# Kernel optimization log

Hardware: AMD Instinct MI355X
Metric: run time of the kernel (lower is better)

Reference implementation:

```python
import jax, jax.numpy as jnp
import numpy as np


def lut_quantize(v, lut):
    """Nearest-neighbor LUT quantization with straight-through estimator.
    lut is sorted ascending; uses searchsorted (no [N, L] blowup)."""
    L = lut.shape[0]
    idx = jnp.clip(jnp.searchsorted(lut, v), 1, L - 1)
    left = jnp.take(lut, idx - 1)
    right = jnp.take(lut, idx)
    q = jnp.where(v - left <= right - v, left, right)
    return v + jax.lax.stop_gradient(q - v)


def mem_conv(x, w, b, lut):
    # memConv2d: weights/bias snapped to LUT levels, then standard 3x3 SAME conv (NCHW/OIHW)
    wq = lut_quantize(w, lut)
    bq = lut_quantize(b, lut)
    y = jax.lax.conv_general_dilated(x, wq, window_strides=(1, 1),
                                     padding=((1, 1), (1, 1)),
                                     dimension_numbers=('NCHW', 'OIHW', 'NCHW'))
    return y + bq[None, :, None, None]


def mem_linear(x, w, b, lut):
    # memLinear: torch-style weight (out, in)
    return x @ lut_quantize(w, lut).T + lut_quantize(b, lut)


def mem_relu(x, lut):
    # memReLu: ReLU followed by LUT quantization of the activation
    return lut_quantize(jnp.maximum(x, 0.0), lut)


def max_pool_2x2(x):
    return jax.lax.reduce_window(x, -jnp.inf, jax.lax.max,
                                 (1, 1, 2, 2), (1, 1, 2, 2), 'VALID')


def _forward(x, lut, w1, b1, w2, b2, w3, b3, w4, b4, w5, b5, w6, b6,
             fw1, fb1, fw2, fb2, fw3, fb3):
    x = mem_relu(mem_conv(x, w1, b1, lut), lut)
    x = mem_relu(mem_conv(x, w2, b2, lut), lut)
    x = max_pool_2x2(x)                      # [B,32,16,16]
    x = mem_relu(mem_conv(x, w3, b3, lut), lut)
    x = mem_relu(mem_conv(x, w4, b4, lut), lut)
    x = max_pool_2x2(x)                      # [B,64,8,8]
    x = mem_relu(mem_conv(x, w5, b5, lut), lut)
    x = mem_relu(mem_conv(x, w6, b6, lut), lut)
    x = max_pool_2x2(x)                      # [B,128,4,4]
    x = x.reshape(-1, 128 * 4 * 4)
    x = mem_relu(mem_linear(x, fw1, fb1, lut), lut)
    x = mem_relu(mem_linear(x, fw2, fb2, lut), lut)
    x = mem_linear(x, fw3, fb3, lut)
    return jax.nn.softmax(x, axis=1)


def setup_inputs() -> dict:
    key = jax.random.key(0)
    ks = jax.random.split(key, 20)
    B = 512
    lut = jnp.linspace(-4.0, 4.0, 129).astype(jnp.float32)

    def conv_w(k, co, ci):
        scale = np.sqrt(2.0 / (ci * 9)).astype(np.float32)
        return jax.random.normal(k, (co, ci, 3, 3), jnp.float32) * scale

    def lin_w(k, co, ci):
        scale = np.sqrt(2.0 / ci).astype(np.float32)
        return jax.random.normal(k, (co, ci), jnp.float32) * scale

    return {
        'x': jax.random.normal(ks[0], (B, 3, 32, 32), jnp.float32),
        'lut': lut,
        'w1': conv_w(ks[1], 32, 3),   'b1': jnp.zeros((32,), jnp.float32),
        'w2': conv_w(ks[2], 32, 32),  'b2': jnp.zeros((32,), jnp.float32),
        'w3': conv_w(ks[3], 64, 32),  'b3': jnp.zeros((64,), jnp.float32),
        'w4': conv_w(ks[4], 64, 64),  'b4': jnp.zeros((64,), jnp.float32),
        'w5': conv_w(ks[5], 128, 64), 'b5': jnp.zeros((128,), jnp.float32),
        'w6': conv_w(ks[6], 128, 128),'b6': jnp.zeros((128,), jnp.float32),
        'fw1': lin_w(ks[7], 512, 2048), 'fb1': jnp.zeros((512,), jnp.float32),
        'fw2': lin_w(ks[8], 128, 512),  'fb2': jnp.zeros((128,), jnp.float32),
        'fw3': lin_w(ks[9], 10, 128),   'fb3': jnp.zeros((10,), jnp.float32),
    }


def reference(x, lut, w1, b1, w2, b2, w3, b3, w4, b4, w5, b5, w6, b6,
              fw1, fb1, fw2, fb2, fw3, fb3):
    return _forward(x, lut, w1, b1, w2, b2, w3, b3, w4, b4, w5, b5, w6, b6,
                    fw1, fb1, fw2, fb2, fw3, fb3)
```

## Files before the change

kernel.cpp:

```cpp
#include <hip/hip_runtime.h>
#include <cstddef>


#define B_SZ 512
typedef unsigned int u32;
typedef __attribute__((ext_vector_type(4))) int i32x4;

__device__ __forceinline__ float lutq(float v) {
    float k = ceilf(v * 16.0f - 0.5f);
    k = fminf(64.0f, fmaxf(-64.0f, k));
    return k * 0.0625f;
}
__device__ __forceinline__ int kq(float x) {
    float kf = ceilf(x * 16.0f - 0.5f);
    kf = fminf(64.0f, fmaxf(-64.0f, kf));
    return (int)kf;
}
__device__ __forceinline__ u32 bmax4u(u32 a, u32 b) {
    u32 r = 0;
    #pragma unroll
    for (int j = 0; j < 4; ++j) {
        u32 x = (a >> (8 * j)) & 255u, y = (b >> (8 * j)) & 255u;
        r |= (x > y ? x : y) << (8 * j);
    }
    return r;
}

__device__ __forceinline__ void prep_conv_frag(const float* __restrict__ w, char* __restrict__ q,
                                               int i, int CI) {
    int NSTEP = (9 * CI + 63) / 64;
    int e = i & 15, t = i >> 4;
    int ln = t & 63, t2 = t >> 6;
    int s = t2 % NSTEP, co_tile = t2 / NSTEP;
    int k = s * 64 + ((ln >> 4) << 4) + e;
    int tap = k / CI, ci = k % CI;
    int co = co_tile * 16 + (ln & 15);
    int val = 0;
    if (tap < 9) val = kq(w[(co * CI + ci) * 9 + tap]);
    q[i] = (char)val;
}
__device__ __forceinline__ void prep_fc_frag(const float* __restrict__ w, char* __restrict__ q,
                                             int i, int K) {
    int S = K >> 6;
    int e = i & 15, t = i >> 4;
    int ln = t & 63, t2 = t >> 6;
    int s = t2 % S, n_tile = t2 / S;
    int n = n_tile * 16 + (ln & 15);
    int k = s * 64 + ((ln >> 4) << 4) + e;
    q[i] = (char)kq(w[(size_t)n * K + k]);
}

__global__ __launch_bounds__(256) void prep_weights(
    const float* __restrict__ w2, const float* __restrict__ w3, const float* __restrict__ w4,
    const float* __restrict__ w5, const float* __restrict__ w6,
    const float* __restrict__ fw1, const float* __restrict__ fw2,
    char* q2, char* q3, char* q4, char* q5, char* q6, char* qf1, char* qf2)
{
    int i = blockIdx.x * 256 + threadIdx.x;
    if (i < 10240)                  { prep_conv_frag(w2, q2, i, 32);  }
    else if ((i -= 10240) < 20480)  { prep_conv_frag(w3, q3, i, 32);  }
    else if ((i -= 20480) < 36864)  { prep_conv_frag(w4, q4, i, 64);  }
    else if ((i -= 36864) < 73728)  { prep_conv_frag(w5, q5, i, 64);  }
    else if ((i -= 73728) < 147456) { prep_conv_frag(w6, q6, i, 128); }
    else if ((i -= 147456) < 1048576){ prep_fc_frag(fw1, qf1, i, 2048); }
    else if ((i -= 1048576) < 65536) { prep_fc_frag(fw2, qf2, i, 512);  }
}

__global__ __launch_bounds__(256) void conv1_mem(
    const float* __restrict__ x, const float* __restrict__ w,
    const float* __restrict__ bias, char* __restrict__ out)
{
    __shared__ float s_w[3][9][16];
    __shared__ float s_b[16];
    __shared__ float s_in[3][10][34];
    const int tid = threadIdx.x;
    const int co0 = blockIdx.y * 16;
    const int b   = blockIdx.x >> 2;
    const int r0  = (blockIdx.x & 3) * 8;
    for (int i = tid; i < 432; i += 256) {
        int o = i % 16, k = (i / 16) % 9, c = i / 144;
        s_w[c][k][o] = lutq(w[((co0 + o) * 3 + c) * 9 + k]);
    }
    if (tid < 16) s_b[tid] = lutq(bias[co0 + tid]);
    for (int i = tid; i < 3 * 10 * 34; i += 256) {
        int xx = i % 34, yy = (i / 34) % 10, c = i / 340;
        int gy = r0 + yy - 1, gx = xx - 1;
        float v = 0.f;
        if ((unsigned)gy < 32u && (unsigned)gx < 32u)
            v = x[(((size_t)b * 3 + c) * 32 + gy) * 32 + gx];
        s_in[c][yy][xx] = v;
    }
    __syncthreads();
    const int y = tid >> 5, xx = tid & 31;
    float acc[16];
    #pragma unroll
    for (int o = 0; o < 16; ++o) acc[o] = 0.f;
    #pragma unroll
    for (int c = 0; c < 3; ++c) {
        #pragma unroll
        for (int k = 0; k < 9; ++k) {
            float iv = s_in[c][y + k / 3][xx + k % 3];
            #pragma unroll
            for (int o = 0; o < 16; ++o) acc[o] = fmaf(iv, s_w[c][k][o], acc[o]);
        }
    }
    u32 u[8];
    #pragma unroll
    for (int j = 0; j < 8; ++j) {
        u32 p = 0;
        #pragma unroll
        for (int q = 0; q < 4; ++q) {
            float v = fmaxf(acc[4 * j + q] + s_b[4 * j + q], 0.f);
            int kk = (int)ceilf(v * 16.0f - 0.5f);
            kk = kk > 64 ? 64 : kk;
            p |= ((u32)kk & 255u) << (8 * q);
        }
        u[j] = p;
    }
    const int p = (b << 10) + ((r0 + y) << 5) + xx;
    u32* o4 = (u32*)(out + (size_t)p * 32 + co0 * 2);
    o4 = (u32*)(out + (size_t)p * 32 + co0);
    #pragma unroll
    for (int j = 0; j < 4; ++j) o4[j] = u[j + 0];
}

template<int HW, int CI, int CO, int RS, int NIMG, int NT, int POOL = 0>
__global__ __launch_bounds__(256) void conv_mfma(
    const char* __restrict__ in,
    const char* __restrict__ wq,
    const float* __restrict__ bias,
    char* __restrict__ out)
{
    constexpr int PH  = HW + 2;
    constexpr int PIX = NIMG * (RS + 2) * PH;
    constexpr int M   = NIMG * RS * HW;
    constexpr int MT  = M / 16;
    constexpr int MW  = MT / 4;
    constexpr int NSTEP = (9 * CI + 63) / 64;
    constexpr int SL  = HW / RS;
    constexpr int NC16 = CI / 16;
    constexpr int NTC = NT * 16;

    __shared__ __align__(128) char s_in[PIX * CI];

    const int tid = threadIdx.x;
    const int g   = blockIdx.x;
    const int b0  = (g / SL) * NIMG;
    const int r0  = (g % SL) * RS;
    const int co0 = blockIdx.y * NTC;

    constexpr int TOTC = PIX * NC16;
    for (int i = tid; i < TOTC; i += 256) {
        int c16 = i % NC16;
        int pp  = i / NC16;
        int xx  = pp % PH;
        int rr  = pp / PH;
        int yy  = rr % (RS + 2);
        int img = rr / (RS + 2);
        int gy = r0 + yy - 1, gx = xx - 1;
        uint4 v = {0u, 0u, 0u, 0u};
        if ((unsigned)gy < (unsigned)HW && (unsigned)gx < (unsigned)HW)
            v = *(const uint4*)(in + ((((size_t)(b0 + img) * HW + gy) * HW + gx) * CI + c16 * 16));
        int off = (pp * CI + c16 * 16) ^ ((pp & 7) << 4);
        *(uint4*)(s_in + off) = v;
    }
    __syncthreads();

    const int wv = tid >> 6, ln = tid & 63;
    const int l15 = ln & 15, lq = ln >> 4;

    int ppad[MW];
    #pragma unroll
    for (int mw = 0; mw < MW; ++mw) {
        int p = (wv * MW + mw) * 16 + l15;
        int img = p / (RS * HW);
        int rem = p % (RS * HW);
        int ly = rem / HW, lx = rem % HW;
        ppad[mw] = (img * (RS + 2) + ly + 1) * PH + lx + 1;
    }

    i32x4 acc[MW][NT] = {};

    const char* wtile = wq + ((size_t)blockIdx.y * NT) * NSTEP * 1024 + (ln << 4);
    auto dp = [](int t) { return (t / 3 - 1) * PH + (t % 3 - 1); };

    #pragma unroll
    for (int s = 0; s < NSTEP; ++s) {
        i32x4 bf[NT];
        #pragma unroll
        for (int nt = 0; nt < NT; ++nt)
            bf[nt] = *(const i32x4*)(wtile + ((nt * NSTEP + s) << 10));
        int dd, ci0;
        if constexpr (CI == 32) {
            int d0 = dp(2 * s);
            int d1 = (2 * s + 1 < 9) ? dp(2 * s + 1) : 0;
            dd  = (lq & 2) ? d1 : d0;
            ci0 = (lq & 1) << 4;
        } else if constexpr (CI == 64) {
            dd  = dp(s);
            ci0 = lq << 4;
        } else {
            dd  = dp(s >> 1);
            ci0 = ((s & 1) << 6) + (lq << 4);
        }
        #pragma unroll
        for (int mw = 0; mw < MW; ++mw) {
            int pix = ppad[mw] + dd;
            int off = (pix * CI + ci0) ^ ((pix & 7) << 4);
            i32x4 af = *(const i32x4*)(s_in + off);
            #pragma unroll
            for (int nt = 0; nt < NT; ++nt)
                acc[mw][nt] = __builtin_amdgcn_mfma_i32_16x16x64_i8(af, bf[nt], acc[mw][nt], 0, 0, 0);
        }
    }

    if constexpr (POOL == 0) {
        #pragma unroll
        for (int nt = 0; nt < NT; ++nt) {
            int kb16 = 16 * kq(bias[co0 + nt * 16 + l15]);
            #pragma unroll
            for (int mw = 0; mw < MW; ++mw) {
                #pragma unroll
                for (int r = 0; r < 4; ++r) {
                    int p = (wv * MW + mw) * 16 + lq * 4 + r;
                    int img = p / (RS * HW), rem = p % (RS * HW);
                    int ly = rem / HW, lx = rem % HW;
                    int vv = acc[mw][nt][r] + kb16;
                    vv = vv > 0 ? vv : 0;
                    int kk = (vv + 7) >> 4;
                    kk = kk > 64 ? 64 : kk;
                    out[(((size_t)(b0 + img) * HW + r0 + ly) * HW + lx) * CO + co0 + nt * 16 + l15] = (char)kk;
                }
            }
        }
    } else {
        __syncthreads();
        char* s_out = s_in;
        #pragma unroll
        for (int nt = 0; nt < NT; ++nt) {
            int kb16 = 16 * kq(bias[co0 + nt * 16 + l15]);
            #pragma unroll
            for (int mw = 0; mw < MW; ++mw) {
                #pragma unroll
                for (int r = 0; r < 4; ++r) {
                    int p = (wv * MW + mw) * 16 + lq * 4 + r;
                    int vv = acc[mw][nt][r] + kb16;
                    vv = vv > 0 ? vv : 0;
                    int kk = (vv + 7) >> 4;
                    kk = kk > 64 ? 64 : kk;
                    s_out[p * NTC + nt * 16 + l15] = (char)kk;
                }
            }
        }
        __syncthreads();
        constexpr int PR = RS / 2, PC = HW / 2, HOW = HW / 2;
        constexpr int OCT = NIMG * PR * PC * (NTC / 16);
        for (int idx = tid; idx < OCT; idx += 256) {
            int c16 = idx % (NTC / 16);
            int pp  = idx / (NTC / 16);
            int xo = pp % PC, yo = (pp / PC) % PR, img = pp / (PC * PR);
            int pb = (img * RS + 2 * yo) * HW + 2 * xo;
            uint4 v0 = *(const uint4*)(s_out + (pb)          * NTC + c16 * 16);
            uint4 v1 = *(const uint4*)(s_out + (pb + 1)      * NTC + c16 * 16);
            uint4 v2 = *(const uint4*)(s_out + (pb + HW)     * NTC + c16 * 16);
            uint4 v3 = *(const uint4*)(s_out + (pb + HW + 1) * NTC + c16 * 16);
            uint4 r;
            r.x = bmax4u(bmax4u(v0.x, v1.x), bmax4u(v2.x, v3.x));
            r.y = bmax4u(bmax4u(v0.y, v1.y), bmax4u(v2.y, v3.y));
            r.z = bmax4u(bmax4u(v0.z, v1.z), bmax4u(v2.z, v3.z));
            r.w = bmax4u(bmax4u(v0.w, v1.w), bmax4u(v2.w, v3.w));
            if constexpr (POOL == 1) {
                *(uint4*)(out + ((((size_t)(b0 + img) * HOW + (r0 >> 1) + yo) * HOW + xo) * CO
                                 + co0 + c16 * 16)) = r;
            } else {
                const char* rv = (const char*)&r;
                #pragma unroll
                for (int j = 0; j < 16; ++j)
                    out[((size_t)(b0 + img) * CO + co0 + c16 * 16 + j) * (PR * PC) + yo * PC + xo] = rv[j];
            }
        }
    }
}

template<int N, int K, int SK>
__global__ __launch_bounds__(256) void fc_splitk(
    const char* __restrict__ x, const char* __restrict__ wq, int* __restrict__ part)
{
    constexpr int KCH = K / SK;
    const int tid = threadIdx.x, wv = tid >> 6, ln = tid & 63;
    const int l15 = ln & 15, lq = ln >> 4;
    const int m0 = blockIdx.x * 128, n0 = blockIdx.y * 128;
    const int kb = blockIdx.z * KCH;
    const int mq = (wv >> 1) * 4, nq = (wv & 1) * 4;
    i32x4 acc[4][4] = {};
    const char* xr[4];
    const char* wt[4];
    #pragma unroll
    for (int t = 0; t < 4; ++t) {
        xr[t] = x  + (size_t)(m0 + (mq + t) * 16 + l15) * K + kb + lq * 16;
        wt[t] = wq + (size_t)((n0 >> 4) + nq + t) * (K / 64) * 1024 + (ln << 4);
    }
    for (int k0 = 0; k0 < KCH; k0 += 64) {
        const int s = (kb + k0) >> 6;
        i32x4 a[4], b[4];
        #pragma unroll
        for (int t = 0; t < 4; ++t) {
            a[t] = *(const i32x4*)(xr[t] + k0);
            b[t] = *(const i32x4*)(wt[t] + (s << 10));
        }
        #pragma unroll
        for (int i = 0; i < 4; ++i)
            #pragma unroll
            for (int j = 0; j < 4; ++j)
                acc[i][j] = __builtin_amdgcn_mfma_i32_16x16x64_i8(a[i], b[j], acc[i][j], 0, 0, 0);
    }
    int* pb = part + (size_t)blockIdx.z * (B_SZ * N);
    #pragma unroll
    for (int j = 0; j < 4; ++j) {
        int n = n0 + (nq + j) * 16 + l15;
        #pragma unroll
        for (int i = 0; i < 4; ++i)
            #pragma unroll
            for (int r = 0; r < 4; ++r) {
                int m = m0 + (mq + i) * 16 + lq * 4 + r;
                pb[(size_t)m * N + n] = acc[i][j][r];
            }
    }
}

template<int N, int SK>
__global__ __launch_bounds__(256) void fc_reduce(
    const int* __restrict__ part, const float* __restrict__ bias, char* __restrict__ out)
{
    int i = blockIdx.x * 256 + threadIdx.x;
    if (i >= B_SZ * N) return;
    int s = 0;
    #pragma unroll
    for (int k = 0; k < SK; ++k) s += part[(size_t)k * (B_SZ * N) + i];
    int vv = s + 16 * kq(bias[i % N]);
    vv = vv > 0 ? vv : 0;
    int kk = (vv + 7) >> 4;
    kk = kk > 64 ? 64 : kk;
    out[i] = (char)kk;
}

__global__ __launch_bounds__(64) void fc3_softmax(
    const char* __restrict__ x, const float* __restrict__ w,
    const float* __restrict__ bias, float* __restrict__ out)
{
    const int r = blockIdx.x;
    const int l = threadIdx.x;
    const float x0 = 0.0625f * (float)x[(size_t)r * 128 + l];
    const float x1 = 0.0625f * (float)x[(size_t)r * 128 + 64 + l];
    float d[10];
    #pragma unroll
    for (int o = 0; o < 10; ++o) {
        float p = x0 * lutq(w[o * 128 + l]) + x1 * lutq(w[o * 128 + 64 + l]);
        #pragma unroll
        for (int s = 32; s > 0; s >>= 1) p += __shfl_xor(p, s);
        d[o] = p + lutq(bias[o]);
    }
    float m = d[0];
    #pragma unroll
    for (int o = 1; o < 10; ++o) m = fmaxf(m, d[o]);
    float sum = 0.f;
    float e[10];
    #pragma unroll
    for (int o = 0; o < 10; ++o) { e[o] = expf(d[o] - m); sum += e[o]; }
    if (l < 10) {
        float num = 0.f;
        #pragma unroll
        for (int o = 0; o < 10; ++o) if (l == o) num = e[o];
        out[(size_t)r * 10 + l] = num / sum;
    }
}

extern "C" void kernel_launch(void* const* d_in, const int* in_sizes, int n_in,
                              void* d_out, int out_size, void* d_ws, size_t ws_size,
                              hipStream_t stream)
{
    const float* x   = (const float*)d_in[0];
    const float* w1  = (const float*)d_in[2];
    const float* b1  = (const float*)d_in[3];
    const float* w2  = (const float*)d_in[4];
    const float* b2  = (const float*)d_in[5];
    const float* w3  = (const float*)d_in[6];
    const float* b3  = (const float*)d_in[7];
    const float* w4  = (const float*)d_in[8];
    const float* b4  = (const float*)d_in[9];
    const float* w5  = (const float*)d_in[10];
    const float* b5  = (const float*)d_in[11];
    const float* w6  = (const float*)d_in[12];
    const float* b6  = (const float*)d_in[13];
    const float* fw1 = (const float*)d_in[14];
    const float* fb1 = (const float*)d_in[15];
    const float* fw2 = (const float*)d_in[16];
    const float* fb2 = (const float*)d_in[17];
    const float* fw3 = (const float*)d_in[18];
    const float* fb3 = (const float*)d_in[19];
    float* out = (float*)d_out;

    char* bufA = (char*)d_ws;
    char* bufB = bufA + (16u << 20);
    char* q2  = bufB + (16u << 20);
    char* q3  = q2 + 10240;
    char* q4  = q3 + 20480;
    char* q5  = q4 + 36864;
    char* q6  = q5 + 73728;
    char* qf1 = q6 + 147456;
    char* qf2 = qf1 + 1048576;
    int*  part = (int*)(qf2 + 65536);
    char* fc1out = (char*)part + (16u << 20);
    char* fc2out = fc1out + 262144;

    dim3 blk(256);

    prep_weights<<<dim3((1402880 + 255) / 256), blk, 0, stream>>>(
        w2, w3, w4, w5, w6, fw1, fw2, q2, q3, q4, q5, q6, qf1, qf2);

    conv1_mem<<<dim3(2048, 2), blk, 0, stream>>>(x, w1, b1, bufA);
    conv_mfma<32, 32, 32, 8, 1, 2, 1><<<dim3(2048, 1), blk, 0, stream>>>(bufA, q2, b2, bufB);
    conv_mfma<16, 32, 64, 16, 1, 4, 0><<<dim3(512, 1), blk, 0, stream>>>(bufB, q3, b3, bufA);
    conv_mfma<16, 64, 64, 16, 1, 4, 1><<<dim3(512, 1), blk, 0, stream>>>(bufA, q4, b4, bufB);
    conv_mfma<8, 64, 128, 8, 2, 4, 0><<<dim3(256, 2), blk, 0, stream>>>(bufB, q5, b5, bufA);
    conv_mfma<8, 128, 128, 8, 2, 4, 2><<<dim3(256, 2), blk, 0, stream>>>(bufA, q6, b6, bufB);

    fc_splitk<512, 2048, 16><<<dim3(4, 4, 16), blk, 0, stream>>>(bufB, qf1, part);
    fc_reduce<512, 16><<<dim3(1024), blk, 0, stream>>>(part, fb1, fc1out);
    fc_splitk<128, 512, 8><<<dim3(4, 1, 8), blk, 0, stream>>>(fc1out, qf2, part);
    fc_reduce<128, 8><<<dim3(256), blk, 0, stream>>>(part, fb2, fc2out);
    fc3_softmax<<<dim3(512), dim3(64), 0, stream>>>(fc2out, fw3, fb3, out);
}
```

Measured before the change: 100.6 us.

## Fuse FC2, FC3 and softmax; emit MFMA-fragment layout from conv6

conv1 now computes all 32 output channels per block, so the input tile is loaded once instead of twice. The last conv writes its pooled output directly in the MFMA A-fragment layout, letting the FC1 kernel read fragments contiguously like the weights. FC2, its reduction, FC3 and softmax are merged into one kernel using shared memory with XOR swizzle, which removes three launches and the split-K partial round trip. In exchange, conv1 has twice the accumulator registers, and the fused tail runs on only 16 blocks.

```diff
diff --git a/kernel.cpp b/kernel.cpp
--- a/kernel.cpp
+++ b/kernel.cpp
@@ -70,18 +70,17 @@
     const float* __restrict__ x, const float* __restrict__ w,
     const float* __restrict__ bias, char* __restrict__ out)
 {
-    __shared__ float s_w[3][9][16];
-    __shared__ float s_b[16];
+    __shared__ float s_w[3][9][32];
+    __shared__ float s_b[32];
     __shared__ float s_in[3][10][34];
     const int tid = threadIdx.x;
-    const int co0 = blockIdx.y * 16;
     const int b   = blockIdx.x >> 2;
     const int r0  = (blockIdx.x & 3) * 8;
-    for (int i = tid; i < 432; i += 256) {
-        int o = i % 16, k = (i / 16) % 9, c = i / 144;
-        s_w[c][k][o] = lutq(w[((co0 + o) * 3 + c) * 9 + k]);
-    }
-    if (tid < 16) s_b[tid] = lutq(bias[co0 + tid]);
+    for (int i = tid; i < 864; i += 256) {
+        int o = i % 32, k = (i / 32) % 9, c = i / 288;
+        s_w[c][k][o] = lutq(w[(o * 3 + c) * 9 + k]);
+    }
+    if (tid < 32) s_b[tid] = lutq(bias[tid]);
     for (int i = tid; i < 3 * 10 * 34; i += 256) {
         int xx = i % 34, yy = (i / 34) % 10, c = i / 340;
         int gy = r0 + yy - 1, gx = xx - 1;
@@ -92,16 +91,16 @@
     }
     __syncthreads();
     const int y = tid >> 5, xx = tid & 31;
-    float acc[16];
-    #pragma unroll
-    for (int o = 0; o < 16; ++o) acc[o] = 0.f;
+    float acc[32];
+    #pragma unroll
+    for (int o = 0; o < 32; ++o) acc[o] = 0.f;
     #pragma unroll
     for (int c = 0; c < 3; ++c) {
         #pragma unroll
         for (int k = 0; k < 9; ++k) {
             float iv = s_in[c][y + k / 3][xx + k % 3];
             #pragma unroll
-            for (int o = 0; o < 16; ++o) acc[o] = fmaf(iv, s_w[c][k][o], acc[o]);
+            for (int o = 0; o < 32; ++o) acc[o] = fmaf(iv, s_w[c][k][o], acc[o]);
         }
     }
     u32 u[8];
@@ -118,10 +117,9 @@
         u[j] = p;
     }
     const int p = (b << 10) + ((r0 + y) << 5) + xx;
-    u32* o4 = (u32*)(out + (size_t)p * 32 + co0 * 2);
-    o4 = (u32*)(out + (size_t)p * 32 + co0);
-    #pragma unroll
-    for (int j = 0; j < 4; ++j) o4[j] = u[j + 0];
+    u32* o4 = (u32*)(out + (size_t)p * 32);
+    #pragma unroll
+    for (int j = 0; j < 8; ++j) o4[j] = u[j];
 }
 
 template<int HW, int CI, int CO, int RS, int NIMG, int NT, int POOL = 0>
@@ -274,19 +272,26 @@
                                  + co0 + c16 * 16)) = r;
             } else {
                 const char* rv = (const char*)&r;
+                int m = b0 + img;
                 #pragma unroll
-                for (int j = 0; j < 16; ++j)
-                    out[((size_t)(b0 + img) * CO + co0 + c16 * 16 + j) * (PR * PC) + yo * PC + xo] = rv[j];
+                for (int j = 0; j < 16; ++j) {
+                    int c = co0 + c16 * 16 + j;
+                    int k = c * 16 + yo * 4 + xo;
+                    int off = (((m >> 4) * 32 + (k >> 6)) << 10)
+                            + ((((k >> 4) & 3) * 16 + (m & 15)) << 4) + (k & 15);
+                    out[off] = rv[j];
+                }
             }
         }
     }
 }
 
 template<int N, int K, int SK>
-__global__ __launch_bounds__(256) void fc_splitk(
-    const char* __restrict__ x, const char* __restrict__ wq, int* __restrict__ part)
+__global__ __launch_bounds__(256) void fc1_splitk(
+    const char* __restrict__ xa, const char* __restrict__ wq, int* __restrict__ part)
 {
     constexpr int KCH = K / SK;
+    constexpr int KS = K / 64;
     const int tid = threadIdx.x, wv = tid >> 6, ln = tid & 63;
     const int l15 = ln & 15, lq = ln >> 4;
     const int m0 = blockIdx.x * 128, n0 = blockIdx.y * 128;
@@ -297,15 +302,15 @@
     const char* wt[4];
     #pragma unroll
     for (int t = 0; t < 4; ++t) {
-        xr[t] = x  + (size_t)(m0 + (mq + t) * 16 + l15) * K + kb + lq * 16;
-        wt[t] = wq + (size_t)((n0 >> 4) + nq + t) * (K / 64) * 1024 + (ln << 4);
+        xr[t] = xa + (size_t)((m0 >> 4) + mq + t) * KS * 1024 + (ln << 4);
+        wt[t] = wq + (size_t)((n0 >> 4) + nq + t) * KS * 1024 + (ln << 4);
     }
     for (int k0 = 0; k0 < KCH; k0 += 64) {
         const int s = (kb + k0) >> 6;
         i32x4 a[4], b[4];
         #pragma unroll
         for (int t = 0; t < 4; ++t) {
-            a[t] = *(const i32x4*)(xr[t] + k0);
+            a[t] = *(const i32x4*)(xr[t] + (s << 10));
             b[t] = *(const i32x4*)(wt[t] + (s << 10));
         }
         #pragma unroll
@@ -344,34 +349,93 @@
     out[i] = (char)kk;
 }
 
-__global__ __launch_bounds__(64) void fc3_softmax(
-    const char* __restrict__ x, const float* __restrict__ w,
-    const float* __restrict__ bias, float* __restrict__ out)
-{
-    const int r = blockIdx.x;
-    const int l = threadIdx.x;
-    const float x0 = 0.0625f * (float)x[(size_t)r * 128 + l];
-    const float x1 = 0.0625f * (float)x[(size_t)r * 128 + 64 + l];
-    float d[10];
-    #pragma unroll
-    for (int o = 0; o < 10; ++o) {
-        float p = x0 * lutq(w[o * 128 + l]) + x1 * lutq(w[o * 128 + 64 + l]);
-        #pragma unroll
-        for (int s = 32; s > 0; s >>= 1) p += __shfl_xor(p, s);
-        d[o] = p + lutq(bias[o]);
-    }
-    float m = d[0];
-    #pragma unroll
-    for (int o = 1; o < 10; ++o) m = fmaxf(m, d[o]);
-    float sum = 0.f;
-    float e[10];
-    #pragma unroll
-    for (int o = 0; o < 10; ++o) { e[o] = expf(d[o] - m); sum += e[o]; }
-    if (l < 10) {
-        float num = 0.f;
-        #pragma unroll
-        for (int o = 0; o < 10; ++o) if (l == o) num = e[o];
-        out[(size_t)r * 10 + l] = num / sum;
+__global__ __launch_bounds__(256) void fc_tail(
+    const char* __restrict__ x, const char* __restrict__ qf2,
+    const float* __restrict__ fb2, const float* __restrict__ fw3,
+    const float* __restrict__ fb3, float* __restrict__ out)
+{
+    __shared__ __align__(16) char sx[32 * 512];
+    __shared__ __align__(16) char sy[32 * 128];
+    __shared__ __align__(16) char sw3[10 * 128];
+    __shared__ float sb3[10];
+    __shared__ int sp[32][8][10];
+
+    const int tid = threadIdx.x;
+    const int m0 = blockIdx.x * 32;
+
+    for (int idx = tid; idx < 1024; idx += 256) {
+        int r = idx >> 5, c16 = idx & 31;
+        uint4 v = *(const uint4*)(x + (size_t)(m0 + r) * 512 + c16 * 16);
+        *(uint4*)(sx + ((r * 512 + c16 * 16) ^ ((r & 7) << 4))) = v;
+    }
+    for (int i = tid; i < 1280; i += 256) sw3[i] = (char)kq(fw3[i]);
+    if (tid < 10) sb3[tid] = lutq(fb3[tid]);
+    __syncthreads();
+
+    const int wv = tid >> 6, ln = tid & 63, l15 = ln & 15, lq = ln >> 4;
+    const int mt = wv >> 1, ntg = (wv & 1) * 4;
+    i32x4 acc[4] = {};
+    #pragma unroll
+    for (int s = 0; s < 8; ++s) {
+        int row = mt * 16 + l15;
+        i32x4 a = *(const i32x4*)(sx + ((row * 512 + s * 64 + lq * 16) ^ ((row & 7) << 4)));
+        #pragma unroll
+        for (int nt = 0; nt < 4; ++nt) {
+            i32x4 b = *(const i32x4*)(qf2 + (((ntg + nt) * 8 + s) << 10) + (ln << 4));
+            acc[nt] = __builtin_amdgcn_mfma_i32_16x16x64_i8(a, b, acc[nt], 0, 0, 0);
+        }
+    }
+    #pragma unroll
+    for (int nt = 0; nt < 4; ++nt) {
+        int n = (ntg + nt) * 16 + l15;
+        int kb16 = 16 * kq(fb2[n]);
+        #pragma unroll
+        for (int r = 0; r < 4; ++r) {
+            int row = mt * 16 + lq * 4 + r;
+            int vv = acc[nt][r] + kb16;
+            vv = vv > 0 ? vv : 0;
+            int kk = (vv + 7) >> 4;
+            kk = kk > 64 ? 64 : kk;
+            sy[(row * 128 + n) ^ ((row & 7) << 4)] = (char)kk;
+        }
+    }
+    __syncthreads();
+
+    {
+        int r = tid >> 3, g = tid & 7;
+        uint4 yv = *(const uint4*)(sy + ((r * 128 + g * 16) ^ ((r & 7) << 4)));
+        const char* yb = (const char*)&yv;
+        #pragma unroll
+        for (int o = 0; o < 10; ++o) {
+            uint4 wv4 = *(const uint4*)(sw3 + o * 128 + g * 16);
+            const char* wb = (const char*)&wv4;
+            int S = 0;
+            #pragma unroll
+            for (int e = 0; e < 16; ++e) S += (int)yb[e] * (int)wb[e];
+            sp[r][g][o] = S;
+        }
+    }
+    __syncthreads();
+
+    if (tid < 32) {
+        int r = tid;
+        float d[10];
+        #pragma unroll
+        for (int o = 0; o < 10; ++o) {
+            int S = 0;
+            #pragma unroll
+            for (int g = 0; g < 8; ++g) S += sp[r][g][o];
+            d[o] = (float)S * 0.00390625f + sb3[o];
+        }
+        float m = d[0];
+        #pragma unroll
+        for (int o = 1; o < 10; ++o) m = fmaxf(m, d[o]);
+        float e[10];
+        float sum = 0.f;
+        #pragma unroll
+        for (int o = 0; o < 10; ++o) { e[o] = expf(d[o] - m); sum += e[o]; }
+        #pragma unroll
+        for (int o = 0; o < 10; ++o) out[(size_t)(m0 + r) * 10 + o] = e[o] / sum;
     }
 }
 
@@ -411,23 +475,21 @@
     char* qf2 = qf1 + 1048576;
     int*  part = (int*)(qf2 + 65536);
     char* fc1out = (char*)part + (16u << 20);
-    char* fc2out = fc1out + 262144;
+    char* fc1a   = fc1out + 262144;
 
     dim3 blk(256);
 
     prep_weights<<<dim3((1402880 + 255) / 256), blk, 0, stream>>>(
         w2, w3, w4, w5, w6, fw1, fw2, q2, q3, q4, q5, q6, qf1, qf2);
 
-    conv1_mem<<<dim3(2048, 2), blk, 0, stream>>>(x, w1, b1, bufA);
+    conv1_mem<<<dim3(2048), blk, 0, stream>>>(x, w1, b1, bufA);
     conv_mfma<32, 32, 32, 8, 1, 2, 1><<<dim3(2048, 1), blk, 0, stream>>>(bufA, q2, b2, bufB);
     conv_mfma<16, 32, 64, 16, 1, 4, 0><<<dim3(512, 1), blk, 0, stream>>>(bufB, q3, b3, bufA);
     conv_mfma<16, 64, 64, 16, 1, 4, 1><<<dim3(512, 1), blk, 0, stream>>>(bufA, q4, b4, bufB);
     conv_mfma<8, 64, 128, 8, 2, 4, 0><<<dim3(256, 2), blk, 0, stream>>>(bufB, q5, b5, bufA);
-    conv_mfma<8, 128, 128, 8, 2, 4, 2><<<dim3(256, 2), blk, 0, stream>>>(bufA, q6, b6, bufB);
-
-    fc_splitk<512, 2048, 16><<<dim3(4, 4, 16), blk, 0, stream>>>(bufB, qf1, part);
+    conv_mfma<8, 128, 128, 8, 2, 4, 2><<<dim3(256, 2), blk, 0, stream>>>(bufA, q6, b6, fc1a);
+
+    fc1_splitk<512, 2048, 16><<<dim3(4, 4, 16), blk, 0, stream>>>(fc1a, qf1, part);
     fc_reduce<512, 16><<<dim3(1024), blk, 0, stream>>>(part, fb1, fc1out);
-    fc_splitk<128, 512, 8><<<dim3(4, 1, 8), blk, 0, stream>>>(fc1out, qf2, part);
-    fc_reduce<128, 8><<<dim3(256), blk, 0, stream>>>(part, fb2, fc2out);
-    fc3_softmax<<<dim3(512), dim3(64), 0, stream>>>(fc2out, fw3, fb3, out);
-}
+    fc_tail<<<dim3(16), blk, 0, stream>>>(fc1out, qf2, fb2, fw3, fb3, out);
+}
```

Result: faster. 97.62 us (-2.9%).
